# Optimization experiments

Measured on AMD Instinct MI355X. Metric: run time of the kernel, lower is better.

The kernel has to match this reference:

```python
import jax, jax.numpy as jnp
import numpy as np

N, T, E = 50000, 12, 800000
IN_DIM, SP_DIM, TP_DIM = 128, 128, 128


def setup_inputs() -> dict:
    key = jax.random.key(0)
    ks = jax.random.split(key, 9)
    h = jax.random.normal(ks[0], (N, T, IN_DIM), dtype=jnp.float32)
    src = jax.random.randint(ks[1], (E,), 0, N, dtype=jnp.int32)
    dst = jax.random.randint(ks[2], (E,), 0, N, dtype=jnp.int32)
    s = 1.0 / np.sqrt(IN_DIM).astype(np.float32)
    # GraphConv layer weights (xavier-ish) and zero biases, layer1: in->sp, layer2: sp->sp
    Wg1 = jax.random.normal(ks[3], (IN_DIM, SP_DIM), dtype=jnp.float32) * s
    bg1 = jnp.zeros((SP_DIM,), jnp.float32)
    Wg2 = jax.random.normal(ks[4], (SP_DIM, SP_DIM), dtype=jnp.float32) * s
    bg2 = jnp.zeros((SP_DIM,), jnp.float32)
    # LSTM params, torch layout: [4H, in]/[4H, H], gate order i,f,g,o
    t = 1.0 / np.sqrt(TP_DIM).astype(np.float32)
    w_ih = jax.random.uniform(ks[5], (4 * TP_DIM, IN_DIM), jnp.float32, -t, t)
    w_hh = jax.random.uniform(ks[6], (4 * TP_DIM, TP_DIM), jnp.float32, -t, t)
    b_ih = jax.random.uniform(ks[7], (4 * TP_DIM,), jnp.float32, -t, t)
    b_hh = jax.random.uniform(ks[8], (4 * TP_DIM,), jnp.float32, -t, t)
    return dict(h=h, src=src, dst=dst, Wg1=Wg1, bg1=bg1, Wg2=Wg2, bg2=bg2,
                w_ih=w_ih, w_hh=w_hh, b_ih=b_ih, b_hh=b_hh)


def _graph_conv(x, src, dst, norm_src, norm_dst, W, b):
    # DGL GraphConv norm='both': D_out^{-1/2} on source feats, sum-aggregate to dst,
    # D_in^{-1/2} on result, then dense weight + bias.
    x = x * norm_src                                  # [N, D]
    m = jax.ops.segment_sum(x[src], dst, num_segments=N)  # SpMM: [N, D]
    m = m * norm_dst
    return m @ W + b


def reference(h, src, dst, Wg1, bg1, Wg2, bg2, w_ih, w_hh, b_ih, b_hh):
    ones_e = jnp.ones((E,), jnp.float32)
    out_deg = jnp.maximum(jax.ops.segment_sum(ones_e, src, num_segments=N), 1.0)
    in_deg = jnp.maximum(jax.ops.segment_sum(ones_e, dst, num_segments=N), 1.0)
    norm_src = (out_deg ** -0.5)[:, None]
    norm_dst = (in_deg ** -0.5)[:, None]

    hs_list = []
    for i in range(T):  # fixed small time horizon
        x = h[:, i]  # [N, IN_DIM]
        x = jax.nn.gelu(_graph_conv(x, src, dst, norm_src, norm_dst, Wg1, bg1), approximate=False)
        x = jax.nn.gelu(_graph_conv(x, src, dst, norm_src, norm_dst, Wg2, bg2), approximate=False)
        hs_list.append(jnp.mean(x, axis=0))  # dgl.mean_nodes over the single graph
    hs = jnp.stack(hs_list, axis=0)[None]  # [1, T, SP_DIM]

    # temporal branch: LSTM over time, nodes as batch, then mean over time
    def lstm_step(carry, x_t):
        hp, cp = carry
        gates = x_t @ w_ih.T + b_ih + hp @ w_hh.T + b_hh  # [N, 4H]
        i_, f_, g_, o_ = jnp.split(gates, 4, axis=-1)
        c = jax.nn.sigmoid(f_) * cp + jax.nn.sigmoid(i_) * jnp.tanh(g_)
        ho = jax.nn.sigmoid(o_) * jnp.tanh(c)
        return (ho, c), ho

    h0 = jnp.zeros((N, TP_DIM), jnp.float32)
    _, ht_seq = jax.lax.scan(lstm_step, (h0, h0), jnp.swapaxes(h, 0, 1))  # [T, N, H]
    ht = jnp.mean(ht_seq, axis=0)  # torch.mean over dim=1 (time) -> [N, H]
    return hs, ht
```

## Files before the change

kernel.cpp:

```cpp
#include <hip/hip_runtime.h>
#include <math.h>

#define NN 50000
#define TT 12
#define EE 800000
#define DIM 128

typedef short bf16x8 __attribute__((ext_vector_type(8)));
typedef float f32x4 __attribute__((ext_vector_type(4)));

__device__ __forceinline__ float sigmoidf_(float x) { return 1.0f / (1.0f + expf(-x)); }
__device__ __forceinline__ float geluf_(float x) {
  return 0.5f * x * (1.0f + erff(x * 0.70710678118654752440f));
}
__device__ __forceinline__ unsigned short f2b(float f) {
  union { float f; unsigned u; } v;
  v.f = f;
  unsigned r = (v.u + 0x7fffu + ((v.u >> 16) & 1u)) >> 16;
  return (unsigned short)r;
}
__device__ __forceinline__ float blo(unsigned u) {
  union { unsigned x; float f; } v; v.x = u << 16; return v.f;
}
__device__ __forceinline__ float bhi(unsigned u) {
  union { unsigned x; float f; } v; v.x = u & 0xffff0000u; return v.f;
}
__device__ __forceinline__ float b2f(unsigned short b) {
  union { unsigned u; float f; } v; v.u = ((unsigned)b) << 16; return v.f;
}


__global__ void deg_kernel(const int* __restrict__ src, const int* __restrict__ dst,
                           int* __restrict__ ds, int* __restrict__ dd) {
  int e = blockIdx.x * 256 + threadIdx.x;
  if (e < EE) {
    atomicAdd(&ds[src[e]], 1);
    atomicAdd(&dd[dst[e]], 1);
  }
}

__global__ void norm_kernel(const int* __restrict__ ds, const int* __restrict__ dd,
                            float* __restrict__ ns, float* __restrict__ nd) {
  int i = blockIdx.x * 256 + threadIdx.x;
  if (i < NN) {
    ns[i] = rsqrtf((float)(ds[i] > 1 ? ds[i] : 1));
    nd[i] = rsqrtf((float)(dd[i] > 1 ? dd[i] : 1));
  }
}

__global__ void scan_kernel(const int* __restrict__ cnt, int* __restrict__ row_ptr, int n) {
  __shared__ int sm[1024];
  __shared__ int carry;
  int tid = threadIdx.x;
  if (tid == 0) carry = 0;
  __syncthreads();
  for (int base = 0; base < n; base += 1024) {
    int v = (base + tid < n) ? cnt[base + tid] : 0;
    sm[tid] = v;
    __syncthreads();
    for (int off = 1; off < 1024; off <<= 1) {
      int t = (tid >= off) ? sm[tid - off] : 0;
      __syncthreads();
      sm[tid] += t;
      __syncthreads();
    }
    int incl = sm[tid];
    if (base + tid < n) row_ptr[base + tid] = carry + incl - v;
    int tot = sm[1023];
    __syncthreads();
    if (tid == 0) carry += tot;
    __syncthreads();
  }
  if (tid == 0) row_ptr[n] = carry;
}

__global__ void csr_kernel(const int* __restrict__ src, const int* __restrict__ dst,
                           const int* __restrict__ row_ptr, int* __restrict__ fill,
                           int* __restrict__ col) {
  int e = blockIdx.x * 256 + threadIdx.x;
  if (e < EE) {
    int d = dst[e];
    int pos = row_ptr[d] + atomicAdd(&fill[d], 1);
    col[pos] = src[e];
  }
}


__global__ void prep_w(const float* __restrict__ Wg1, const float* __restrict__ Wg2,
                       const float* __restrict__ wih, const float* __restrict__ whh,
                       const float* __restrict__ bih, const float* __restrict__ bhh,
                       unsigned short* __restrict__ W1bt, unsigned short* __restrict__ W2bt,
                       unsigned short* __restrict__ Bc, float* __restrict__ bgate) {
  int i = blockIdx.x * 256 + threadIdx.x;
  if (i < 16384) {
    int n = i >> 7, k = i & 127;
    W1bt[n * 128 + k] = f2b(Wg1[k * 128 + n]);
    W2bt[n * 128 + k] = f2b(Wg2[k * 128 + n]);
  }
  int j = i - 16384;
  if (j >= 0 && j < 131072) {
    int n = j >> 8, k = j & 255;
    Bc[j] = f2b(k < 128 ? wih[n * 128 + k] : whh[n * 128 + (k - 128)]);
  }
  if (i < 512) bgate[i] = bih[i] + bhh[i];
}

#define LDT 40

__global__ __launch_bounds__(256) void gemm_scaleA_f32(
    const float* __restrict__ A, const float* __restrict__ ns,
    const unsigned short* __restrict__ Bt, unsigned short* __restrict__ C, int M) {
  __shared__ unsigned short As[128 * LDT];
  __shared__ unsigned short Bs[128 * LDT];
  const int tid = threadIdx.x;
  const int lane = tid & 63, wid = tid >> 6;
  const int quad = lane >> 4, l16 = lane & 15;
  const int row0 = blockIdx.x * 128;
  const int wm = (wid >> 1) * 64, wn = (wid & 1) * 64;
  f32x4 acc[4][4] = {};
  for (int k0 = 0; k0 < 128; k0 += 32) {
#pragma unroll
    for (int rds = 0; rds < 2; rds++) {
      int idx = (rds * 256 + tid) * 8;
      int m = idx >> 5, c = idx & 31;
      int gr = row0 + m;
      if (gr >= M) gr = M - 1;
      float s = ns[gr / TT];
      const float4 va = *(const float4*)(A + (size_t)gr * 128 + k0 + c);
      const float4 vb = *(const float4*)(A + (size_t)gr * 128 + k0 + c + 4);
      unsigned short* d = &As[m * LDT + c];
      d[0] = f2b(va.x * s); d[1] = f2b(va.y * s); d[2] = f2b(va.z * s); d[3] = f2b(va.w * s);
      d[4] = f2b(vb.x * s); d[5] = f2b(vb.y * s); d[6] = f2b(vb.z * s); d[7] = f2b(vb.w * s);
      *(uint4*)(&Bs[m * LDT + c]) = *(const uint4*)(Bt + m * 128 + k0 + c);
    }
    __syncthreads();
    bf16x8 af[4], bfr[4];
#pragma unroll
    for (int im = 0; im < 4; im++)
      af[im] = *(const bf16x8*)(&As[(wm + im * 16 + l16) * LDT + quad * 8]);
#pragma unroll
    for (int in = 0; in < 4; in++)
      bfr[in] = *(const bf16x8*)(&Bs[(wn + in * 16 + l16) * LDT + quad * 8]);
#pragma unroll
    for (int im = 0; im < 4; im++)
#pragma unroll
      for (int in = 0; in < 4; in++)
        acc[im][in] = __builtin_amdgcn_mfma_f32_16x16x32_bf16(af[im], bfr[in], acc[im][in], 0, 0, 0);
    __syncthreads();
  }
#pragma unroll
  for (int im = 0; im < 4; im++)
#pragma unroll
    for (int r = 0; r < 4; r++) {
      int row = row0 + wm + im * 16 + quad * 4 + r;
      if (row < M)
#pragma unroll
        for (int in = 0; in < 4; in++)
          C[(size_t)row * 128 + wn + in * 16 + l16] = f2b(acc[im][in][r]);
    }
}

__global__ __launch_bounds__(256) void gemm_bf16A(
    const unsigned short* __restrict__ A, const unsigned short* __restrict__ Bt,
    unsigned short* __restrict__ C, int M) {
  __shared__ unsigned short As[128 * LDT];
  __shared__ unsigned short Bs[128 * LDT];
  const int tid = threadIdx.x;
  const int lane = tid & 63, wid = tid >> 6;
  const int quad = lane >> 4, l16 = lane & 15;
  const int row0 = blockIdx.x * 128;
  const int wm = (wid >> 1) * 64, wn = (wid & 1) * 64;
  f32x4 acc[4][4] = {};
  for (int k0 = 0; k0 < 128; k0 += 32) {
#pragma unroll
    for (int rds = 0; rds < 2; rds++) {
      int idx = (rds * 256 + tid) * 8;
      int m = idx >> 5, c = idx & 31;
      int gr = row0 + m;
      if (gr >= M) gr = M - 1;
      *(uint4*)(&As[m * LDT + c]) = *(const uint4*)(A + (size_t)gr * 128 + k0 + c);
      *(uint4*)(&Bs[m * LDT + c]) = *(const uint4*)(Bt + m * 128 + k0 + c);
    }
    __syncthreads();
    bf16x8 af[4], bfr[4];
#pragma unroll
    for (int im = 0; im < 4; im++)
      af[im] = *(const bf16x8*)(&As[(wm + im * 16 + l16) * LDT + quad * 8]);
#pragma unroll
    for (int in = 0; in < 4; in++)
      bfr[in] = *(const bf16x8*)(&Bs[(wn + in * 16 + l16) * LDT + quad * 8]);
#pragma unroll
    for (int im = 0; im < 4; im++)
#pragma unroll
      for (int in = 0; in < 4; in++)
        acc[im][in] = __builtin_amdgcn_mfma_f32_16x16x32_bf16(af[im], bfr[in], acc[im][in], 0, 0, 0);
    __syncthreads();
  }
#pragma unroll
  for (int im = 0; im < 4; im++)
#pragma unroll
    for (int r = 0; r < 4; r++) {
      int row = row0 + wm + im * 16 + quad * 4 + r;
      if (row < M)
#pragma unroll
        for (int in = 0; in < 4; in++)
          C[(size_t)row * 128 + wn + in * 16 + l16] = f2b(acc[im][in][r]);
    }
}

template <bool SCALE_OUT>
__global__ __launch_bounds__(256) void spmm_b(
    const unsigned short* __restrict__ z, const int* __restrict__ rowp,
    const int* __restrict__ colx, const float* __restrict__ ns,
    const float* __restrict__ nd, const float* __restrict__ bg,
    unsigned short* __restrict__ y) {
  int d = (blockIdx.x * 256 + threadIdx.x) >> 6;
  int lane = threadIdx.x & 63;
  if (d >= NN) return;
  int beg = rowp[d], end = rowp[d + 1];
  float acc[3][8] = {};
  int j = beg;
  int s = (j < end) ? colx[j] : 0;
  while (j < end) {
    int snext = (j + 1 < end) ? colx[j + 1] : 0;
    const unsigned short* base = z + (size_t)s * 1536 + lane * 8;
#pragma unroll
    for (int r = 0; r < 3; r++) {
      uint4 v = *(const uint4*)(base + r * 512);
      acc[r][0] += blo(v.x); acc[r][1] += bhi(v.x);
      acc[r][2] += blo(v.y); acc[r][3] += bhi(v.y);
      acc[r][4] += blo(v.z); acc[r][5] += bhi(v.z);
      acc[r][6] += blo(v.w); acc[r][7] += bhi(v.w);
    }
    s = snext;
    j++;
  }
  float scn = nd[d];
  float sco = SCALE_OUT ? ns[d] : 1.0f;
  float bgv[8];
#pragma unroll
  for (int k = 0; k < 8; k++) bgv[k] = bg[(lane * 8 + k) & 127];
  unsigned short* outp = y + (size_t)d * 1536 + lane * 8;
#pragma unroll
  for (int r = 0; r < 3; r++) {
    unsigned short o[8];
#pragma unroll
    for (int k = 0; k < 8; k++)
      o[k] = f2b(sco * geluf_(acc[r][k] * scn + bgv[k]));
    *(uint4*)(outp + r * 512) = *(const uint4*)o;
  }
}


__global__ void colmean_b(const unsigned short* __restrict__ x, float* __restrict__ out) {
  int t = blockIdx.x;
  int cc = threadIdx.x & 127;
  int half = threadIdx.x >> 7;
  float s = 0.f;
  for (int n = blockIdx.y * 2 + half; n < NN; n += 64)
    s += b2f(x[((size_t)n * TT + t) * 128 + cc]);
  __shared__ float sm[256];
  sm[threadIdx.x] = s;
  __syncthreads();
  if (threadIdx.x < 128)
    atomicAdd(&out[t * 128 + cc], (sm[threadIdx.x] + sm[threadIdx.x + 128]) * (1.0f / NN));
}

#define HPLD 132

__global__ __launch_bounds__(512, 2) void lstm_all(
    const float* __restrict__ h, const unsigned short* __restrict__ Bc,
    const float* __restrict__ bgate, float* __restrict__ ht_out, int M) {
  __shared__ unsigned short As[64 * LDT];
  __shared__ unsigned short Bs[512 * LDT];
  __shared__ unsigned short Hp[64 * HPLD];
  const int tid = threadIdx.x;
  const int lane = tid & 63, w = tid >> 6;
  const int quad = lane >> 4, l16 = lane & 15;
  const int row0 = blockIdx.x * 64;
  const int colg = w * 16 + l16;

  float cs[4][4], hacc[4][4];
#pragma unroll
  for (int im = 0; im < 4; im++)
#pragma unroll
    for (int r = 0; r < 4; r++) { cs[im][r] = 0.f; hacc[im][r] = 0.f; }

  for (int i = tid; i < 64 * HPLD / 2; i += 512) ((unsigned*)Hp)[i] = 0u;

  const float bi = bgate[colg], bff = bgate[128 + colg];
  const float bgg = bgate[256 + colg], bo = bgate[384 + colg];
  __syncthreads();

  for (int t = 0; t < TT; t++) {
    f32x4 acc[4][4] = {};
    for (int k0 = 0; k0 < 256; k0 += 32) {
      if (k0 < 128) {
        int idx = tid * 4;
        int m = idx >> 5, c = idx & 31;
        int gr = row0 + m;
        if (gr >= M) gr = M - 1;
        const float4 va = *(const float4*)(h + ((size_t)gr * TT + t) * 128 + k0 + c);
        unsigned short tmp[4] = {f2b(va.x), f2b(va.y), f2b(va.z), f2b(va.w)};
        *(uint2*)(&As[m * LDT + c]) = *(const uint2*)tmp;
      }
#pragma unroll
      for (int it = 0; it < 4; it++) {
        int jj = (it * 512 + tid) * 8;
        int n = jj >> 5, cc = jj & 31;
        *(uint4*)(&Bs[n * LDT + cc]) = *(const uint4*)(Bc + (size_t)n * 256 + k0 + cc);
      }
      __syncthreads();
      bf16x8 af[4];
      if (k0 < 128) {
#pragma unroll
        for (int im = 0; im < 4; im++)
          af[im] = *(const bf16x8*)(&As[(im * 16 + l16) * LDT + quad * 8]);
      } else {
#pragma unroll
        for (int im = 0; im < 4; im++)
          af[im] = *(const bf16x8*)(&Hp[(im * 16 + l16) * HPLD + (k0 - 128) + quad * 8]);
      }
#pragma unroll
      for (int g = 0; g < 4; g++) {
        bf16x8 bf = *(const bf16x8*)(&Bs[(g * 128 + colg) * LDT + quad * 8]);
#pragma unroll
        for (int im = 0; im < 4; im++)
          acc[im][g] = __builtin_amdgcn_mfma_f32_16x16x32_bf16(af[im], bf, acc[im][g], 0, 0, 0);
      }
      __syncthreads();
    }
#pragma unroll
    for (int im = 0; im < 4; im++)
#pragma unroll
      for (int r = 0; r < 4; r++) {
        float iv = sigmoidf_(acc[im][0][r] + bi);
        float fv = sigmoidf_(acc[im][1][r] + bff);
        float gv = tanhf(acc[im][2][r] + bgg);
        float ov = sigmoidf_(acc[im][3][r] + bo);
        float cn = fv * cs[im][r] + iv * gv;
        cs[im][r] = cn;
        float ho = ov * tanhf(cn);
        hacc[im][r] += ho;
        Hp[(im * 16 + quad * 4 + r) * HPLD + colg] = f2b(ho);
      }
    __syncthreads();
  }
#pragma unroll
  for (int im = 0; im < 4; im++)
#pragma unroll
    for (int r = 0; r < 4; r++) {
      int gr = row0 + im * 16 + quad * 4 + r;
      if (gr < M) ht_out[(size_t)gr * 128 + colg] = hacc[im][r] * (1.0f / TT);
    }
}


extern "C" void kernel_launch(void* const* d_in, const int* in_sizes, int n_in,
                              void* d_out, int out_size, void* d_ws, size_t ws_size,
                              hipStream_t stream) {
  const float* h   = (const float*)d_in[0];
  const int*   src = (const int*)d_in[1];
  const int*   dst = (const int*)d_in[2];
  const float* Wg1 = (const float*)d_in[3];
  const float* bg1 = (const float*)d_in[4];
  const float* Wg2 = (const float*)d_in[5];
  const float* bg2 = (const float*)d_in[6];
  const float* wih = (const float*)d_in[7];
  const float* whh = (const float*)d_in[8];
  const float* bih = (const float*)d_in[9];
  const float* bhh = (const float*)d_in[10];

  float* out = (float*)d_out;
  float* hs_out = out;
  float* ht_out = out + TT * DIM;

  char* p = (char*)d_ws;
  auto alloc = [&](size_t bytes) -> void* {
    void* r = (void*)p;
    p += (bytes + 255) & ~(size_t)255;
    return r;
  };
  const size_t MB = (size_t)NN * TT * DIM;
  unsigned short* bufA = (unsigned short*)alloc(MB * 2);
  unsigned short* bufB = (unsigned short*)alloc(MB * 2);
  unsigned short* W1bt = (unsigned short*)alloc(16384 * 2);
  unsigned short* W2bt = (unsigned short*)alloc(16384 * 2);
  unsigned short* Bc   = (unsigned short*)alloc(131072 * 2);
  float* bgate = (float*)alloc(512 * 4);
  float* ns    = (float*)alloc(NN * 4);
  float* nd    = (float*)alloc(NN * 4);
  int* degs    = (int*)alloc(NN * 4);
  int* degd    = (int*)alloc(NN * 4);
  int* rowp    = (int*)alloc((NN + 1) * 4);
  int* colx    = (int*)alloc(EE * 4);

  hipMemsetAsync(degs, 0, NN * 4, stream);
  hipMemsetAsync(degd, 0, NN * 4, stream);
  hipMemsetAsync(hs_out, 0, TT * DIM * 4, stream);

  deg_kernel<<<(EE + 255) / 256, 256, 0, stream>>>(src, dst, degs, degd);
  norm_kernel<<<(NN + 255) / 256, 256, 0, stream>>>(degs, degd, ns, nd);
  scan_kernel<<<1, 1024, 0, stream>>>(degd, rowp, NN);
  hipMemsetAsync(degs, 0, NN * 4, stream);
  csr_kernel<<<(EE + 255) / 256, 256, 0, stream>>>(src, dst, rowp, degs, colx);
  prep_w<<<(16384 + 131072 + 255) / 256, 256, 0, stream>>>(Wg1, Wg2, wih, whh, bih, bhh,
                                                            W1bt, W2bt, Bc, bgate);

  const int M = NN * TT;
  const int gblocks = (M + 127) / 128;
  const int sblocks = (NN + 3) / 4;

  gemm_scaleA_f32<<<gblocks, 256, 0, stream>>>(h, ns, W1bt, bufA, M);
  spmm_b<true><<<sblocks, 256, 0, stream>>>(bufA, rowp, colx, ns, nd, bg1, bufB);
  gemm_bf16A<<<gblocks, 256, 0, stream>>>(bufB, W2bt, bufA, M);
  spmm_b<false><<<sblocks, 256, 0, stream>>>(bufA, rowp, colx, ns, nd, bg2, bufB);
  colmean_b<<<dim3(TT, 32), 256, 0, stream>>>(bufB, hs_out);

  lstm_all<<<(NN + 63) / 64, 512, 0, stream>>>(h, Bc, bgate, ht_out, NN);
}
```

Baseline: 2.566 ms.

## Hoist LSTM input projection into fused h GEMM and keep W_hh in LDS

Computes the LSTM input gates x_t·W_ih for all timesteps in the first GraphConv GEMM, which already reads h, using a 5-column-block grid. The results go to an fp16 gate buffer that is interleaved per column. The LSTM kernel now loads W_hh into shared memory once, skips the hidden matmul at t=0, and does only a K=128 recurrent matmul per step. The node-norm scale moves from the A operand to the output epilogue. In exchange it writes and reads back a large 600k×512 fp16 intermediate with strided 2-byte stores. The large LDS footprint may also cut LSTM occupancy.

Measured after the change: 2.881 ms. +12.3%, slower.

```diff
diff --git a/kernel.cpp b/kernel.cpp
--- a/kernel.cpp
+++ b/kernel.cpp
@@ -27,6 +27,12 @@
 }
 __device__ __forceinline__ float b2f(unsigned short b) {
   union { unsigned u; float f; } v; v.u = ((unsigned)b) << 16; return v.f;
+}
+__device__ __forceinline__ unsigned short f2h(float f) {
+  union { _Float16 h; unsigned short s; } v; v.h = (_Float16)f; return v.s;
+}
+__device__ __forceinline__ float h2f(unsigned u) {
+  union { unsigned short s; _Float16 h; } v; v.s = (unsigned short)u; return (float)v.h;
 }
 
 
@@ -89,33 +95,37 @@
 __global__ void prep_w(const float* __restrict__ Wg1, const float* __restrict__ Wg2,
                        const float* __restrict__ wih, const float* __restrict__ whh,
                        const float* __restrict__ bih, const float* __restrict__ bhh,
-                       unsigned short* __restrict__ W1bt, unsigned short* __restrict__ W2bt,
-                       unsigned short* __restrict__ Bc, float* __restrict__ bgate) {
+                       unsigned short* __restrict__ W2bt, unsigned short* __restrict__ Wcomb,
+                       unsigned short* __restrict__ whhb, float* __restrict__ bgate) {
   int i = blockIdx.x * 256 + threadIdx.x;
   if (i < 16384) {
     int n = i >> 7, k = i & 127;
-    W1bt[n * 128 + k] = f2b(Wg1[k * 128 + n]);
-    W2bt[n * 128 + k] = f2b(Wg2[k * 128 + n]);
+    W2bt[i] = f2b(Wg2[k * 128 + n]);
   }
   int j = i - 16384;
-  if (j >= 0 && j < 131072) {
-    int n = j >> 8, k = j & 255;
-    Bc[j] = f2b(k < 128 ? wih[n * 128 + k] : whh[n * 128 + (k - 128)]);
-  }
+  if (j >= 0 && j < 81920) {
+    int n = j >> 7, k = j & 127;
+    Wcomb[j] = f2b(n < 128 ? Wg1[k * 128 + n] : wih[(n - 128) * 128 + k]);
+  }
+  int q = i - (16384 + 81920);
+  if (q >= 0 && q < 65536) whhb[q] = f2b(whh[q]);
   if (i < 512) bgate[i] = bih[i] + bhh[i];
 }
 
 #define LDT 40
 
-__global__ __launch_bounds__(256) void gemm_scaleA_f32(
+__global__ __launch_bounds__(256) void gemm_h_fused(
     const float* __restrict__ A, const float* __restrict__ ns,
-    const unsigned short* __restrict__ Bt, unsigned short* __restrict__ C, int M) {
+    const unsigned short* __restrict__ Wcomb, unsigned short* __restrict__ C,
+    unsigned short* __restrict__ xg, int M) {
   __shared__ unsigned short As[128 * LDT];
   __shared__ unsigned short Bs[128 * LDT];
+  const int cb = blockIdx.x;
+  const unsigned short* Bt = Wcomb + cb * 16384;
   const int tid = threadIdx.x;
   const int lane = tid & 63, wid = tid >> 6;
   const int quad = lane >> 4, l16 = lane & 15;
-  const int row0 = blockIdx.x * 128;
+  const int row0 = blockIdx.y * 128;
   const int wm = (wid >> 1) * 64, wn = (wid & 1) * 64;
   f32x4 acc[4][4] = {};
   for (int k0 = 0; k0 < 128; k0 += 32) {
@@ -125,12 +135,11 @@
       int m = idx >> 5, c = idx & 31;
       int gr = row0 + m;
       if (gr >= M) gr = M - 1;
-      float s = ns[gr / TT];
       const float4 va = *(const float4*)(A + (size_t)gr * 128 + k0 + c);
       const float4 vb = *(const float4*)(A + (size_t)gr * 128 + k0 + c + 4);
       unsigned short* d = &As[m * LDT + c];
-      d[0] = f2b(va.x * s); d[1] = f2b(va.y * s); d[2] = f2b(va.z * s); d[3] = f2b(va.w * s);
-      d[4] = f2b(vb.x * s); d[5] = f2b(vb.y * s); d[6] = f2b(vb.z * s); d[7] = f2b(vb.w * s);
+      d[0] = f2b(va.x); d[1] = f2b(va.y); d[2] = f2b(va.z); d[3] = f2b(va.w);
+      d[4] = f2b(vb.x); d[5] = f2b(vb.y); d[6] = f2b(vb.z); d[7] = f2b(vb.w);
       *(uint4*)(&Bs[m * LDT + c]) = *(const uint4*)(Bt + m * 128 + k0 + c);
     }
     __syncthreads();
@@ -148,16 +157,34 @@
         acc[im][in] = __builtin_amdgcn_mfma_f32_16x16x32_bf16(af[im], bfr[in], acc[im][in], 0, 0, 0);
     __syncthreads();
   }
-#pragma unroll
-  for (int im = 0; im < 4; im++)
-#pragma unroll
-    for (int r = 0; r < 4; r++) {
-      int row = row0 + wm + im * 16 + quad * 4 + r;
-      if (row < M)
-#pragma unroll
-        for (int in = 0; in < 4; in++)
-          C[(size_t)row * 128 + wn + in * 16 + l16] = f2b(acc[im][in][r]);
-    }
+  if (cb == 0) {
+#pragma unroll
+    for (int im = 0; im < 4; im++)
+#pragma unroll
+      for (int r = 0; r < 4; r++) {
+        int row = row0 + wm + im * 16 + quad * 4 + r;
+        if (row < M) {
+          float s = ns[row / TT];
+#pragma unroll
+          for (int in = 0; in < 4; in++)
+            C[(size_t)row * 128 + wn + in * 16 + l16] = f2b(acc[im][in][r] * s);
+        }
+      }
+  } else {
+    const int g = cb - 1;
+#pragma unroll
+    for (int im = 0; im < 4; im++)
+#pragma unroll
+      for (int r = 0; r < 4; r++) {
+        int row = row0 + wm + im * 16 + quad * 4 + r;
+        if (row < M)
+#pragma unroll
+          for (int in = 0; in < 4; in++) {
+            int colc = wn + in * 16 + l16;
+            xg[(size_t)row * 512 + colc * 4 + g] = f2h(acc[im][in][r]);
+          }
+      }
+  }
 }
 
 __global__ __launch_bounds__(256) void gemm_bf16A(
@@ -207,6 +234,7 @@
           C[(size_t)row * 128 + wn + in * 16 + l16] = f2b(acc[im][in][r]);
     }
 }
+
 
 template <bool SCALE_OUT>
 __global__ __launch_bounds__(256) void spmm_b(
@@ -266,78 +294,76 @@
     atomicAdd(&out[t * 128 + cc], (sm[threadIdx.x] + sm[threadIdx.x + 128]) * (1.0f / NN));
 }
 
-#define HPLD 132
-
-__global__ __launch_bounds__(512, 2) void lstm_all(
-    const float* __restrict__ h, const unsigned short* __restrict__ Bc,
+#define HPLD 136
+#define WLD 136
+
+__global__ __launch_bounds__(512, 2) void lstm_hh(
+    const unsigned short* __restrict__ whhb, const unsigned short* __restrict__ xg,
     const float* __restrict__ bgate, float* __restrict__ ht_out, int M) {
-  __shared__ unsigned short As[64 * LDT];
-  __shared__ unsigned short Bs[512 * LDT];
+  __shared__ unsigned short Ws[512 * WLD];
   __shared__ unsigned short Hp[64 * HPLD];
   const int tid = threadIdx.x;
-  const int lane = tid & 63, w = tid >> 6;
+  const int lane = tid & 63;
+  const int w = tid >> 6;
   const int quad = lane >> 4, l16 = lane & 15;
   const int row0 = blockIdx.x * 64;
   const int colg = w * 16 + l16;
 
+#pragma unroll
+  for (int it = 0; it < 16; it++) {
+    int idx = it * 512 + tid;
+    int n = idx >> 4, c = (idx & 15) * 8;
+    *(uint4*)(&Ws[n * WLD + c]) = *(const uint4*)(whhb + n * 128 + c);
+  }
+
   float cs[4][4], hacc[4][4];
 #pragma unroll
   for (int im = 0; im < 4; im++)
 #pragma unroll
     for (int r = 0; r < 4; r++) { cs[im][r] = 0.f; hacc[im][r] = 0.f; }
-
-  for (int i = tid; i < 64 * HPLD / 2; i += 512) ((unsigned*)Hp)[i] = 0u;
 
   const float bi = bgate[colg], bff = bgate[128 + colg];
   const float bgg = bgate[256 + colg], bo = bgate[384 + colg];
   __syncthreads();
 
   for (int t = 0; t < TT; t++) {
+    uint2 xv[4][4];
+#pragma unroll
+    for (int im = 0; im < 4; im++)
+#pragma unroll
+      for (int r = 0; r < 4; r++) {
+        int gr = row0 + im * 16 + quad * 4 + r;
+        int grc = gr < M ? gr : M - 1;
+        xv[im][r] = *(const uint2*)(xg + ((size_t)grc * TT + t) * 512 + colg * 4);
+      }
+
     f32x4 acc[4][4] = {};
-    for (int k0 = 0; k0 < 256; k0 += 32) {
-      if (k0 < 128) {
-        int idx = tid * 4;
-        int m = idx >> 5, c = idx & 31;
-        int gr = row0 + m;
-        if (gr >= M) gr = M - 1;
-        const float4 va = *(const float4*)(h + ((size_t)gr * TT + t) * 128 + k0 + c);
-        unsigned short tmp[4] = {f2b(va.x), f2b(va.y), f2b(va.z), f2b(va.w)};
-        *(uint2*)(&As[m * LDT + c]) = *(const uint2*)tmp;
-      }
-#pragma unroll
-      for (int it = 0; it < 4; it++) {
-        int jj = (it * 512 + tid) * 8;
-        int n = jj >> 5, cc = jj & 31;
-        *(uint4*)(&Bs[n * LDT + cc]) = *(const uint4*)(Bc + (size_t)n * 256 + k0 + cc);
+    if (t) {
+#pragma unroll
+      for (int k0 = 0; k0 < 128; k0 += 32) {
+        bf16x8 af[4];
+#pragma unroll
+        for (int im = 0; im < 4; im++)
+          af[im] = *(const bf16x8*)(&Hp[(im * 16 + l16) * HPLD + k0 + quad * 8]);
+#pragma unroll
+        for (int g = 0; g < 4; g++) {
+          bf16x8 bf = *(const bf16x8*)(&Ws[(g * 128 + colg) * WLD + k0 + quad * 8]);
+#pragma unroll
+          for (int im = 0; im < 4; im++)
+            acc[im][g] = __builtin_amdgcn_mfma_f32_16x16x32_bf16(af[im], bf, acc[im][g], 0, 0, 0);
+        }
       }
       __syncthreads();
-      bf16x8 af[4];
-      if (k0 < 128) {
-#pragma unroll
-        for (int im = 0; im < 4; im++)
-          af[im] = *(const bf16x8*)(&As[(im * 16 + l16) * LDT + quad * 8]);
-      } else {
-#pragma unroll
-        for (int im = 0; im < 4; im++)
-          af[im] = *(const bf16x8*)(&Hp[(im * 16 + l16) * HPLD + (k0 - 128) + quad * 8]);
-      }
-#pragma unroll
-      for (int g = 0; g < 4; g++) {
-        bf16x8 bf = *(const bf16x8*)(&Bs[(g * 128 + colg) * LDT + quad * 8]);
-#pragma unroll
-        for (int im = 0; im < 4; im++)
-          acc[im][g] = __builtin_amdgcn_mfma_f32_16x16x32_bf16(af[im], bf, acc[im][g], 0, 0, 0);
-      }
-      __syncthreads();
-    }
+    }
+
 #pragma unroll
     for (int im = 0; im < 4; im++)
 #pragma unroll
       for (int r = 0; r < 4; r++) {
-        float iv = sigmoidf_(acc[im][0][r] + bi);
-        float fv = sigmoidf_(acc[im][1][r] + bff);
-        float gv = tanhf(acc[im][2][r] + bgg);
-        float ov = sigmoidf_(acc[im][3][r] + bo);
+        float iv = sigmoidf_(acc[im][0][r] + h2f(xv[im][r].x & 0xffffu) + bi);
+        float fv = sigmoidf_(acc[im][1][r] + h2f(xv[im][r].x >> 16) + bff);
+        float gv = tanhf(acc[im][2][r] + h2f(xv[im][r].y & 0xffffu) + bgg);
+        float ov = sigmoidf_(acc[im][3][r] + h2f(xv[im][r].y >> 16) + bo);
         float cn = fv * cs[im][r] + iv * gv;
         cs[im][r] = cn;
         float ho = ov * tanhf(cn);
@@ -384,9 +410,10 @@
   const size_t MB = (size_t)NN * TT * DIM;
   unsigned short* bufA = (unsigned short*)alloc(MB * 2);
   unsigned short* bufB = (unsigned short*)alloc(MB * 2);
-  unsigned short* W1bt = (unsigned short*)alloc(16384 * 2);
+  unsigned short* xgb  = (unsigned short*)alloc((size_t)NN * TT * 512 * 2);
   unsigned short* W2bt = (unsigned short*)alloc(16384 * 2);
-  unsigned short* Bc   = (unsigned short*)alloc(131072 * 2);
+  unsigned short* Wcomb= (unsigned short*)alloc(81920 * 2);
+  unsigned short* whhb = (unsigned short*)alloc(65536 * 2);
   float* bgate = (float*)alloc(512 * 4);
   float* ns    = (float*)alloc(NN * 4);
   float* nd    = (float*)alloc(NN * 4);
@@ -404,18 +431,18 @@
   scan_kernel<<<1, 1024, 0, stream>>>(degd, rowp, NN);
   hipMemsetAsync(degs, 0, NN * 4, stream);
   csr_kernel<<<(EE + 255) / 256, 256, 0, stream>>>(src, dst, rowp, degs, colx);
-  prep_w<<<(16384 + 131072 + 255) / 256, 256, 0, stream>>>(Wg1, Wg2, wih, whh, bih, bhh,
-                                                            W1bt, W2bt, Bc, bgate);
+  prep_w<<<(16384 + 81920 + 65536 + 255) / 256, 256, 0, stream>>>(
+      Wg1, Wg2, wih, whh, bih, bhh, W2bt, Wcomb, whhb, bgate);
 
   const int M = NN * TT;
   const int gblocks = (M + 127) / 128;
   const int sblocks = (NN + 3) / 4;
 
-  gemm_scaleA_f32<<<gblocks, 256, 0, stream>>>(h, ns, W1bt, bufA, M);
+  gemm_h_fused<<<dim3(5, gblocks), 256, 0, stream>>>(h, ns, Wcomb, bufA, xgb, M);
   spmm_b<true><<<sblocks, 256, 0, stream>>>(bufA, rowp, colx, ns, nd, bg1, bufB);
   gemm_bf16A<<<gblocks, 256, 0, stream>>>(bufB, W2bt, bufA, M);
   spmm_b<false><<<sblocks, 256, 0, stream>>>(bufA, rowp, colx, ns, nd, bg2, bufB);
   colmean_b<<<dim3(TT, 32), 256, 0, stream>>>(bufB, hs_out);
 
-  lstm_all<<<(NN + 63) / 64, 512, 0, stream>>>(h, Bc, bgate, ht_out, NN);
-}
+  lstm_hh<<<(NN + 63) / 64, 512, 0, stream>>>(whhb, xgb, bgate, ht_out, NN);
+}
```
